# Kernel optimization log

Measured on AMD Instinct MI355X. Metric: run time of the kernel, lower is better.

## Reference

```python
import jax, jax.numpy as jnp
import numpy as np

B, F, H, P, L, A = 8192, 512, 1024, 64, 32, 16


def setup_inputs() -> dict:
    key = jax.random.key(0)
    ks = jax.random.split(key, 7)
    s = lambda k, shape, fan: jax.random.normal(k, shape, jnp.float32) / np.sqrt(fan)
    return {
        "state": jax.random.normal(ks[0], (B, F), jnp.float32),
        "W0": s(ks[1], (A, H, F), F),
        "b0": jnp.zeros((A, H), jnp.float32),
        "W1": s(ks[2], (A, H, H), H),
        "b1": jnp.zeros((A, H), jnp.float32),
        "W2": s(ks[3], (A, P, H), H),
        "ltl_corr": jax.random.normal(ks[4], (A, P), jnp.float32),
        # learned policies = {0..31}; active-only experts = policies 32..47
        "learned_idx": jnp.arange(L, dtype=jnp.int64),
        "active_idx": jnp.arange(L, L + A, dtype=jnp.int64),
    }


def reference(state, W0, b0, W1, b1, W2, ltl_corr, learned_idx, active_idx):
    # Batched over the A active experts (original loops in Python per expert).
    h = jax.nn.relu(jnp.einsum('bf,ahf->abh', state, W0) + b0[:, None, :])   # [A,B,H]
    h = jax.nn.relu(jnp.einsum('abh,agh->abg', h, W1) + b1[:, None, :])      # [A,B,H]
    x = jnp.einsum('abh,aph->abp', h, W2) + ltl_corr[:, None, :]             # [A,B,P]
    # softmax restricted to learned columns, scattered back into zeros
    sub = jax.nn.softmax(x[:, :, learned_idx], axis=-1)                       # [A,B,L]
    emb = jnp.zeros_like(x).at[:, :, learned_idx].set(sub)                    # [A,B,P]
    # all_emb starts as identity per batch element; active rows replaced
    all_emb = jnp.broadcast_to(jnp.eye(P, dtype=state.dtype), (state.shape[0], P, P))
    all_emb = all_emb.at[:, active_idx, :].set(jnp.transpose(emb, (1, 0, 2)))
    return all_emb
```

## Files before the change

### kernel.cpp

```cpp
#include <hip/hip_runtime.h>
#include <hip/hip_bf16.h>


typedef short v8s __attribute__((ext_vector_type(8)));
typedef float v4f __attribute__((ext_vector_type(4)));
using bf16 = __hip_bfloat16;

#define AS_GLOBAL __attribute__((address_space(1)))
#define AS_LDS    __attribute__((address_space(3)))

static constexpr int Mtot = 8192;
static constexpr int Fdim = 512;
static constexpr int Hdim = 1024;
static constexpr int Pdim = 64;
static constexpr int Aexp = 16;

__device__ __forceinline__ void gload_lds16(const void* g, void* l) {
  __builtin_amdgcn_global_load_lds((const AS_GLOBAL void*)g, (AS_LDS void*)l, 16, 0, 0);
}
__device__ __forceinline__ unsigned short bfu(float x) {
  bf16 h = __float2bfloat16(x);
  return *(unsigned short*)&h;
}
#define MFMA16(d, a, b) d = __builtin_amdgcn_mfma_f32_16x16x32_bf16(a, b, d, 0, 0, 0)
#define WAIT_VM3 asm volatile("s_waitcnt vmcnt(3)" ::: "memory")
#define WAIT_VM0 asm volatile("s_waitcnt vmcnt(0)" ::: "memory")
#define BAR() __builtin_amdgcn_s_barrier()

__device__ __forceinline__ void cvt_span(const float* __restrict__ src,
                                         unsigned short* __restrict__ dst, int n4,
                                         int gid, int nthr) {
  for (int i = gid; i < n4; i += nthr) {
    float4 v = ((const float4*)src)[i];
    ushort4 u;
    u.x = bfu(v.x); u.y = bfu(v.y); u.z = bfu(v.z); u.w = bfu(v.w);
    ((ushort4*)dst)[i] = u;
  }
}

__global__ void cvt_all_kernel(const float* __restrict__ s0, unsigned short* __restrict__ d0, int n0,
                               const float* __restrict__ s1, unsigned short* __restrict__ d1, int n1,
                               const float* __restrict__ s2, unsigned short* __restrict__ d2, int n2,
                               const float* __restrict__ s3, unsigned short* __restrict__ d3, int n3) {
  int gid = blockIdx.x * blockDim.x + threadIdx.x;
  int nthr = gridDim.x * blockDim.x;
  cvt_span(s0, d0, n0, gid, nthr);
  cvt_span(s1, d1, n1, gid, nthr);
  cvt_span(s2, d2, n2, gid, nthr);
  cvt_span(s3, d3, n3, gid, nthr);
}

__global__ void ident_kernel(float* __restrict__ outp) {
  const long total4 = (long)Mtot * Pdim * Pdim / 4;
  long i = blockIdx.x * 256 + threadIdx.x;
  const long stride = (long)gridDim.x * 256;
  for (; i < total4; i += stride) {
    long e = i * 4;
    int q = (int)(e & 63);
    int p = (int)((e >> 6) & 63);
    float4 v;
    v.x = (p == q) ? 1.f : 0.f;
    v.y = (p == q + 1) ? 1.f : 0.f;
    v.z = (p == q + 2) ? 1.f : 0.f;
    v.w = (p == q + 3) ? 1.f : 0.f;
    *(float4*)&outp[e] = v;
  }
}

template <int NT>
__global__ __launch_bounds__(256) void gemm97_kernel(
    const bf16* __restrict__ Ain, long aAmul,
    const bf16* __restrict__ Bw,
    const float* __restrict__ bias,
    bf16* __restrict__ Cout, long aCmul, int nbm) {
  constexpr int K = NT * 64;
  __shared__ short lsA[128 * 64];
  __shared__ short lsB[128 * 64];
  const int t = threadIdx.x;
  const int nwg = nbm * 128;

  const int flat = blockIdx.x;
  const int perx = nwg >> 3;
  const int swz = (flat & 7) * perx + (flat >> 3);
  const int perg = nbm * 8;
  const int g = swz / perg;
  const int e = swz % perg;
  const int msup = e >> 5;
  const int ny = (e >> 2) & 7;
  const int mloc = e & 3;
  const int mBase = (msup * 4 + mloc) * 128;
  const int nBase = ny * 128;

  const bf16* A0 = Ain + (size_t)g * aAmul;
  const bf16* B0 = Bw + (size_t)g * (1024 * K);
  const float* biasE = bias + g * 1024 + nBase;
  bf16* C0 = Cout + (size_t)g * aCmul + nBase;

  const int w = t >> 6, lane = t & 63;
  const int wm = w >> 1, wn = w & 1;
  const int lr = lane & 15, lk = lane >> 4;

  v4f acc[4][4];
#pragma unroll
  for (int m = 0; m < 4; ++m)
#pragma unroll
    for (int n = 0; n < 4; ++n) acc[m][n] = (v4f)(0.f);

  const int rowA = t >> 3;
  const int sg = (t & 7) ^ (rowA & 7);
  const bf16* gA = A0 + (size_t)(mBase + rowA) * K + sg * 8;
  const bf16* gB = B0 + (size_t)(nBase + rowA) * K + sg * 8;

  for (int k0 = 0; k0 < K; k0 += 64) {
#pragma unroll
    for (int i = 0; i < 4; ++i) {
      gload_lds16(gA + (size_t)(i * 32) * K + k0, &lsA[i * 2048 + t * 8]);
      gload_lds16(gB + (size_t)(i * 32) * K + k0, &lsB[i * 2048 + t * 8]);
    }
    __syncthreads();
#pragma unroll
    for (int kk = 0; kk < 2; ++kk) {
      v8s af[4], bfr[4];
#pragma unroll
      for (int m = 0; m < 4; ++m) {
        const int row = wm * 64 + m * 16 + lr;
        af[m] = *(const v8s*)&lsA[row * 64 + ((((kk << 2) + lk) ^ (row & 7)) << 3)];
      }
#pragma unroll
      for (int n = 0; n < 4; ++n) {
        const int row = wn * 64 + n * 16 + lr;
        bfr[n] = *(const v8s*)&lsB[row * 64 + ((((kk << 2) + lk) ^ (row & 7)) << 3)];
      }
#pragma unroll
      for (int m = 0; m < 4; ++m)
#pragma unroll
        for (int n = 0; n < 4; ++n)
          MFMA16(acc[m][n], af[m], bfr[n]);
    }
    __syncthreads();
  }

#pragma unroll
  for (int n = 0; n < 4; ++n) {
    const int colIn = wn * 64 + n * 16 + lr;
    const float bv = biasE[colIn];
#pragma unroll
    for (int m = 0; m < 4; ++m) {
      const int row0 = mBase + wm * 64 + m * 16 + lk * 4;
#pragma unroll
      for (int j = 0; j < 4; ++j) {
        float v = acc[m][n][j] + bv;
        v = v > 0.f ? v : 0.f;
        C0[(size_t)(row0 + j) * 1024 + colIn] = __float2bfloat16(v);
      }
    }
  }
}

__global__ __launch_bounds__(256) void gemm2_softmax_kernel(
    const bf16* __restrict__ h1, const bf16* __restrict__ W2b,
    const float* __restrict__ ltl, const int* __restrict__ lidx,
    const int* __restrict__ aidx, float* __restrict__ outp, int mGlobBase, int MC) {
  __shared__ short lsA[2][32 * 64];
  __shared__ short lsB[2][64 * 64];
  __shared__ float X[32][68];
  __shared__ int s_lidx[32];
  __shared__ int s_inv[64];
  __shared__ int s_arow;
  const int a = blockIdx.y;
  const bf16* Ain = h1 + (size_t)a * MC * Hdim;
  const bf16* Bw = W2b + (size_t)a * Pdim * Hdim;
  const float* ltlE = ltl + (size_t)a * Pdim;

  const int t = threadIdx.x;
  const int mBase = blockIdx.x * 32;
  const int w = t >> 6, lane = t & 63;
  const int lr = lane & 15, lk = lane >> 4;
  const int wr = w & 1, wq = w >> 1;

  if (t < 64) s_inv[t] = -1;
  __syncthreads();
  if (t < 32) {
    int q = lidx[t];
    s_lidx[t] = q;
    s_inv[q] = t;
  }
  if (t == 0) s_arow = aidx[a];
  __syncthreads();

  const int srow = t >> 3;
  const int sg = (t & 7) ^ ((t >> 3) & 7);
  const bf16* gA = Ain + (size_t)(mBase + srow) * Hdim + sg * 8;
  const bf16* gB = Bw + (size_t)srow * Hdim + sg * 8;

  auto stage = [&](int buf, int kt) {
    gload_lds16(gA + kt * 64, &lsA[buf][t * 8]);
    gload_lds16(gB + kt * 64, &lsB[buf][t * 8]);
    gload_lds16(gB + (size_t)32 * Hdim + kt * 64, &lsB[buf][2048 + t * 8]);
  };

  v4f acc[2];
  acc[0] = (v4f)(0.f); acc[1] = (v4f)(0.f);

  stage(0, 0);
  for (int kt = 0; kt < 16; ++kt) {
    const int buf = kt & 1;
    if (kt + 1 < 16) { stage(buf ^ 1, kt + 1); WAIT_VM3; } else { WAIT_VM0; }
    BAR();
#pragma unroll
    for (int s = 0; s < 2; ++s) {
      int rowA = wr * 16 + lr;
      v8s af = *(const v8s*)&lsA[buf][rowA * 64 + ((((s << 2) + lk) ^ (rowA & 7)) << 3)];
#pragma unroll
      for (int n = 0; n < 2; ++n) {
        int rowB = wq * 32 + n * 16 + lr;
        v8s bf = *(const v8s*)&lsB[buf][rowB * 64 + ((((s << 2) + lk) ^ (rowB & 7)) << 3)];
        MFMA16(acc[n], af, bf);
      }
    }
    BAR();
  }

#pragma unroll
  for (int n = 0; n < 2; ++n) {
    const int col = wq * 32 + n * 16 + lr;
    const float lc = ltlE[col];
#pragma unroll
    for (int j = 0; j < 4; ++j) {
      X[wr * 16 + lk * 4 + j][col] = acc[n][j] + lc;
    }
  }
  __syncthreads();

  if (t < 32) {
    const int r = t;
    float mx = -1e30f;
#pragma unroll
    for (int l = 0; l < 32; ++l) mx = fmaxf(mx, X[r][s_lidx[l]]);
    float s = 0.f;
#pragma unroll
    for (int l = 0; l < 32; ++l) s += __expf(X[r][s_lidx[l]] - mx);
    const float rs = 1.f / s;
    const size_t obase = ((size_t)(mGlobBase + mBase + r) * 64 + s_arow) * 64;
#pragma unroll
    for (int q0 = 0; q0 < 64; q0 += 4) {
      float4 v;
      v.x = (s_inv[q0 + 0] >= 0) ? __expf(X[r][q0 + 0] - mx) * rs : 0.f;
      v.y = (s_inv[q0 + 1] >= 0) ? __expf(X[r][q0 + 1] - mx) * rs : 0.f;
      v.z = (s_inv[q0 + 2] >= 0) ? __expf(X[r][q0 + 2] - mx) * rs : 0.f;
      v.w = (s_inv[q0 + 3] >= 0) ? __expf(X[r][q0 + 3] - mx) * rs : 0.f;
      *(float4*)&outp[obase + q0] = v;
    }
  }
}

extern "C" void kernel_launch(void* const* d_in, const int* in_sizes, int n_in,
                              void* d_out, int out_size, void* d_ws, size_t ws_size,
                              hipStream_t stream) {
  const float* state = (const float*)d_in[0];
  const float* W0 = (const float*)d_in[1];
  const float* b0 = (const float*)d_in[2];
  const float* W1 = (const float*)d_in[3];
  const float* b1 = (const float*)d_in[4];
  const float* W2 = (const float*)d_in[5];
  const float* ltl = (const float*)d_in[6];
  const int* lidx = (const int*)d_in[7];
  const int* aidx = (const int*)d_in[8];
  float* outp = (float*)d_out;

  char* ws = (char*)d_ws;
  bf16* stateb = (bf16*)ws;
  bf16* W0b = stateb + (size_t)Mtot * Fdim;
  bf16* W1b = W0b + (size_t)Aexp * Hdim * Fdim;
  bf16* W2b = W1b + (size_t)Aexp * Hdim * Hdim;
  bf16* h0 = W2b + (size_t)Aexp * Pdim * Hdim;
  const size_t fixedB = (size_t)(Mtot * Fdim + Aexp * Hdim * Fdim +
                                 Aexp * Hdim * Hdim + Aexp * Pdim * Hdim) * 2;
  int MC = 2048;
  while (MC > 512 && fixedB + (size_t)2 * Aexp * MC * Hdim * 2 + 4096 > ws_size) MC >>= 1;
  bf16* h1 = h0 + (size_t)Aexp * MC * Hdim;

  ident_kernel<<<dim3(4096), dim3(256), 0, stream>>>(outp);
  cvt_all_kernel<<<dim3(2048), dim3(256), 0, stream>>>(
      state, (unsigned short*)stateb, Mtot * Fdim / 4,
      W0, (unsigned short*)W0b, Aexp * Hdim * Fdim / 4,
      W1, (unsigned short*)W1b, Aexp * Hdim * Hdim / 4,
      W2, (unsigned short*)W2b, Aexp * Pdim * Hdim / 4);

  const int nbm = MC / 128;
  for (int mOff = 0; mOff < Mtot; mOff += MC) {
    gemm97_kernel<Fdim / 64><<<dim3(nbm * 128), dim3(256), 0, stream>>>(
        stateb + (size_t)mOff * Fdim, 0L,
        W0b, b0, h0, (long)MC * Hdim, nbm);
    gemm97_kernel<Hdim / 64><<<dim3(nbm * 128), dim3(256), 0, stream>>>(
        h0, (long)MC * Hdim,
        W1b, b1, h1, (long)MC * Hdim, nbm);
    gemm2_softmax_kernel<<<dim3(MC / 32, Aexp), dim3(256), 0, stream>>>(
        h1, W2b, ltl, lidx, aidx, outp, mOff, MC);
  }
}
```

Baseline: 622.5 us.

## Chunk by expert groups instead of batch rows; enlarge gemm2 tile to 128 rows

The host loop now splits the work into groups of G experts covering the full 8192-row batch, where it used to cover all experts over batch chunks. The two large GEMMs now see full-M grids for G experts at a time. The final GEMM+softmax kernel uses 128-row tiles with 2x4 MFMA accumulators per wave and a shared LDS union, so more rows share each W2 tile. The identity fill and the softmax output writes now use nontemporal stores. The gemm97 index math now hardcodes 512 blocks per expert, which ties it to Mtot=8192.

After: 834.9 us. 34.1% more time.

```diff
diff --git a/kernel.cpp b/kernel.cpp
--- a/kernel.cpp
+++ b/kernel.cpp
@@ -23,7 +23,7 @@
   return *(unsigned short*)&h;
 }
 #define MFMA16(d, a, b) d = __builtin_amdgcn_mfma_f32_16x16x32_bf16(a, b, d, 0, 0, 0)
-#define WAIT_VM3 asm volatile("s_waitcnt vmcnt(3)" ::: "memory")
+#define WAIT_VM6 asm volatile("s_waitcnt vmcnt(6)" ::: "memory")
 #define WAIT_VM0 asm volatile("s_waitcnt vmcnt(0)" ::: "memory")
 #define BAR() __builtin_amdgcn_s_barrier()
 
@@ -58,12 +58,12 @@
     long e = i * 4;
     int q = (int)(e & 63);
     int p = (int)((e >> 6) & 63);
-    float4 v;
-    v.x = (p == q) ? 1.f : 0.f;
-    v.y = (p == q + 1) ? 1.f : 0.f;
-    v.z = (p == q + 2) ? 1.f : 0.f;
-    v.w = (p == q + 3) ? 1.f : 0.f;
-    *(float4*)&outp[e] = v;
+    v4f v;
+    v[0] = (p == q) ? 1.f : 0.f;
+    v[1] = (p == q + 1) ? 1.f : 0.f;
+    v[2] = (p == q + 2) ? 1.f : 0.f;
+    v[3] = (p == q + 3) ? 1.f : 0.f;
+    __builtin_nontemporal_store(v, (v4f*)&outp[e]);
   }
 }
 
@@ -72,19 +72,18 @@
     const bf16* __restrict__ Ain, long aAmul,
     const bf16* __restrict__ Bw,
     const float* __restrict__ bias,
-    bf16* __restrict__ Cout, long aCmul, int nbm) {
+    bf16* __restrict__ Cout, long aCmul) {
   constexpr int K = NT * 64;
   __shared__ short lsA[128 * 64];
   __shared__ short lsB[128 * 64];
   const int t = threadIdx.x;
-  const int nwg = nbm * 128;
+  const int nwg = gridDim.x;
 
   const int flat = blockIdx.x;
   const int perx = nwg >> 3;
   const int swz = (flat & 7) * perx + (flat >> 3);
-  const int perg = nbm * 8;
-  const int g = swz / perg;
-  const int e = swz % perg;
+  const int g = swz >> 9;
+  const int e = swz & 511;
   const int msup = e >> 5;
   const int ny = (e >> 2) & 7;
   const int mloc = e & 3;
@@ -160,23 +159,25 @@
 __global__ __launch_bounds__(256) void gemm2_softmax_kernel(
     const bf16* __restrict__ h1, const bf16* __restrict__ W2b,
     const float* __restrict__ ltl, const int* __restrict__ lidx,
-    const int* __restrict__ aidx, float* __restrict__ outp, int mGlobBase, int MC) {
-  __shared__ short lsA[2][32 * 64];
-  __shared__ short lsB[2][64 * 64];
-  __shared__ float X[32][68];
+    const int* __restrict__ aidx, int aOffset, float* __restrict__ outp) {
+  __shared__ char smem[49152];
   __shared__ int s_lidx[32];
   __shared__ int s_inv[64];
   __shared__ int s_arow;
-  const int a = blockIdx.y;
-  const bf16* Ain = h1 + (size_t)a * MC * Hdim;
-  const bf16* Bw = W2b + (size_t)a * Pdim * Hdim;
-  const float* ltlE = ltl + (size_t)a * Pdim;
+  short* lsA = (short*)smem;
+  short* lsB = (short*)(smem + 32768);
+  float(*X)[68] = (float(*)[68])smem;
+
+  const int aLoc = blockIdx.y;
+  const bf16* Ain = h1 + (size_t)aLoc * Mtot * Hdim;
+  const bf16* Bw = W2b + (size_t)aLoc * Pdim * Hdim;
+  const float* ltlE = ltl + (size_t)aLoc * Pdim;
 
   const int t = threadIdx.x;
-  const int mBase = blockIdx.x * 32;
+  const int mBase = blockIdx.x * 128;
   const int w = t >> 6, lane = t & 63;
   const int lr = lane & 15, lk = lane >> 4;
-  const int wr = w & 1, wq = w >> 1;
+  const int wm = w;
 
   if (t < 64) s_inv[t] = -1;
   __syncthreads();
@@ -185,54 +186,69 @@
     s_lidx[t] = q;
     s_inv[q] = t;
   }
-  if (t == 0) s_arow = aidx[a];
+  if (t == 0) s_arow = aidx[aOffset + aLoc];
   __syncthreads();
 
   const int srow = t >> 3;
-  const int sg = (t & 7) ^ ((t >> 3) & 7);
+  const int sg = (t & 7) ^ (srow & 7);
   const bf16* gA = Ain + (size_t)(mBase + srow) * Hdim + sg * 8;
   const bf16* gB = Bw + (size_t)srow * Hdim + sg * 8;
 
   auto stage = [&](int buf, int kt) {
-    gload_lds16(gA + kt * 64, &lsA[buf][t * 8]);
-    gload_lds16(gB + kt * 64, &lsB[buf][t * 8]);
-    gload_lds16(gB + (size_t)32 * Hdim + kt * 64, &lsB[buf][2048 + t * 8]);
+#pragma unroll
+    for (int i = 0; i < 4; ++i)
+      gload_lds16(gA + (size_t)(i * 32) * Hdim + kt * 64, &lsA[buf * 8192 + i * 2048 + t * 8]);
+#pragma unroll
+    for (int i = 0; i < 2; ++i)
+      gload_lds16(gB + (size_t)(i * 32) * Hdim + kt * 64, &lsB[buf * 4096 + i * 2048 + t * 8]);
   };
 
-  v4f acc[2];
-  acc[0] = (v4f)(0.f); acc[1] = (v4f)(0.f);
+  v4f acc[2][4];
+#pragma unroll
+  for (int m = 0; m < 2; ++m)
+#pragma unroll
+    for (int n = 0; n < 4; ++n) acc[m][n] = (v4f)(0.f);
 
   stage(0, 0);
   for (int kt = 0; kt < 16; ++kt) {
     const int buf = kt & 1;
-    if (kt + 1 < 16) { stage(buf ^ 1, kt + 1); WAIT_VM3; } else { WAIT_VM0; }
+    if (kt + 1 < 16) { stage(buf ^ 1, kt + 1); WAIT_VM6; } else { WAIT_VM0; }
     BAR();
 #pragma unroll
-    for (int s = 0; s < 2; ++s) {
-      int rowA = wr * 16 + lr;
-      v8s af = *(const v8s*)&lsA[buf][rowA * 64 + ((((s << 2) + lk) ^ (rowA & 7)) << 3)];
-#pragma unroll
-      for (int n = 0; n < 2; ++n) {
-        int rowB = wq * 32 + n * 16 + lr;
-        v8s bf = *(const v8s*)&lsB[buf][rowB * 64 + ((((s << 2) + lk) ^ (rowB & 7)) << 3)];
-        MFMA16(acc[n], af, bf);
-      }
+    for (int ks = 0; ks < 2; ++ks) {
+      v8s af[2], bfr[4];
+#pragma unroll
+      for (int m = 0; m < 2; ++m) {
+        const int row = wm * 32 + m * 16 + lr;
+        af[m] = *(const v8s*)&lsA[buf * 8192 + row * 64 + ((((ks << 2) + lk) ^ (lr & 7)) << 3)];
+      }
+#pragma unroll
+      for (int n = 0; n < 4; ++n) {
+        const int row = n * 16 + lr;
+        bfr[n] = *(const v8s*)&lsB[buf * 4096 + row * 64 + ((((ks << 2) + lk) ^ (lr & 7)) << 3)];
+      }
+#pragma unroll
+      for (int m = 0; m < 2; ++m)
+#pragma unroll
+        for (int n = 0; n < 4; ++n)
+          MFMA16(acc[m][n], af[m], bfr[n]);
     }
     BAR();
   }
 
 #pragma unroll
-  for (int n = 0; n < 2; ++n) {
-    const int col = wq * 32 + n * 16 + lr;
+  for (int n = 0; n < 4; ++n) {
+    const int col = n * 16 + lr;
     const float lc = ltlE[col];
 #pragma unroll
-    for (int j = 0; j < 4; ++j) {
-      X[wr * 16 + lk * 4 + j][col] = acc[n][j] + lc;
-    }
+    for (int m = 0; m < 2; ++m)
+#pragma unroll
+      for (int j = 0; j < 4; ++j)
+        X[wm * 32 + m * 16 + lk * 4 + j][col] = acc[m][n][j] + lc;
   }
   __syncthreads();
 
-  if (t < 32) {
+  if (t < 128) {
     const int r = t;
     float mx = -1e30f;
 #pragma unroll
@@ -241,15 +257,15 @@
 #pragma unroll
     for (int l = 0; l < 32; ++l) s += __expf(X[r][s_lidx[l]] - mx);
     const float rs = 1.f / s;
-    const size_t obase = ((size_t)(mGlobBase + mBase + r) * 64 + s_arow) * 64;
+    const size_t obase = ((size_t)(mBase + r) * 64 + s_arow) * 64;
 #pragma unroll
     for (int q0 = 0; q0 < 64; q0 += 4) {
-      float4 v;
-      v.x = (s_inv[q0 + 0] >= 0) ? __expf(X[r][q0 + 0] - mx) * rs : 0.f;
-      v.y = (s_inv[q0 + 1] >= 0) ? __expf(X[r][q0 + 1] - mx) * rs : 0.f;
-      v.z = (s_inv[q0 + 2] >= 0) ? __expf(X[r][q0 + 2] - mx) * rs : 0.f;
-      v.w = (s_inv[q0 + 3] >= 0) ? __expf(X[r][q0 + 3] - mx) * rs : 0.f;
-      *(float4*)&outp[obase + q0] = v;
+      v4f v;
+      v[0] = (s_inv[q0 + 0] >= 0) ? __expf(X[r][q0 + 0] - mx) * rs : 0.f;
+      v[1] = (s_inv[q0 + 1] >= 0) ? __expf(X[r][q0 + 1] - mx) * rs : 0.f;
+      v[2] = (s_inv[q0 + 2] >= 0) ? __expf(X[r][q0 + 2] - mx) * rs : 0.f;
+      v[3] = (s_inv[q0 + 3] >= 0) ? __expf(X[r][q0 + 3] - mx) * rs : 0.f;
+      __builtin_nontemporal_store(v, (v4f*)&outp[obase + q0]);
     }
   }
 }
@@ -276,9 +292,10 @@
   bf16* h0 = W2b + (size_t)Aexp * Pdim * Hdim;
   const size_t fixedB = (size_t)(Mtot * Fdim + Aexp * Hdim * Fdim +
                                  Aexp * Hdim * Hdim + Aexp * Pdim * Hdim) * 2;
-  int MC = 2048;
-  while (MC > 512 && fixedB + (size_t)2 * Aexp * MC * Hdim * 2 + 4096 > ws_size) MC >>= 1;
-  bf16* h1 = h0 + (size_t)Aexp * MC * Hdim;
+  int G = 8;
+  while (G > 1 && fixedB + (size_t)2 * G * Mtot * Hdim * 2 + 4096 > ws_size) G >>= 1;
+  bf16* h1 = h0 + (size_t)G * Mtot * Hdim;
+  const int passes = Aexp / G;
 
   ident_kernel<<<dim3(4096), dim3(256), 0, stream>>>(outp);
   cvt_all_kernel<<<dim3(2048), dim3(256), 0, stream>>>(
@@ -287,15 +304,19 @@
       W1, (unsigned short*)W1b, Aexp * Hdim * Hdim / 4,
       W2, (unsigned short*)W2b, Aexp * Pdim * Hdim / 4);
 
-  const int nbm = MC / 128;
-  for (int mOff = 0; mOff < Mtot; mOff += MC) {
-    gemm97_kernel<Fdim / 64><<<dim3(nbm * 128), dim3(256), 0, stream>>>(
-        stateb + (size_t)mOff * Fdim, 0L,
-        W0b, b0, h0, (long)MC * Hdim, nbm);
-    gemm97_kernel<Hdim / 64><<<dim3(nbm * 128), dim3(256), 0, stream>>>(
-        h0, (long)MC * Hdim,
-        W1b, b1, h1, (long)MC * Hdim, nbm);
-    gemm2_softmax_kernel<<<dim3(MC / 32, Aexp), dim3(256), 0, stream>>>(
-        h1, W2b, ltl, lidx, aidx, outp, mOff, MC);
-  }
-}
+  for (int p = 0; p < passes; ++p) {
+    gemm97_kernel<Fdim / 64><<<dim3(512 * G), dim3(256), 0, stream>>>(
+        stateb, 0L,
+        W0b + (size_t)p * G * Hdim * Fdim,
+        b0 + (size_t)p * G * Hdim,
+        h0, (long)Mtot * Hdim);
+    gemm97_kernel<Hdim / 64><<<dim3(512 * G), dim3(256), 0, stream>>>(
+        h0, (long)Mtot * Hdim,
+        W1b + (size_t)p * G * Hdim * Hdim,
+        b1 + (size_t)p * G * Hdim,
+        h1, (long)Mtot * Hdim);
+    gemm2_softmax_kernel<<<dim3(Mtot / 128, G), dim3(256), 0, stream>>>(
+        h1, W2b + (size_t)p * G * Pdim * Hdim,
+        ltl + (size_t)p * G * Pdim, lidx, aidx, p * G, outp);
+  }
+}
```

## Skip identity writes for active rows, use nontemporal stores, enlarge GEMM chunks

Applied to the files above, without the earlier changes.

The identity-fill kernel now builds a bitmask of active expert rows and skips writing those rows, because the softmax kernel overwrites them anyway. Output stores in both kernels become nontemporal. When the workspace is large enough, the first-layer GEMM runs once over the full batch and the second layer plus softmax run in larger chunks, which cuts launch count and improves occupancy per launch. The cost is a larger workspace for the full h0 buffer, and the skip relies on the active index list being read correctly in every thread.

After: 816.2 us. 1.31x slower.

```diff
diff --git a/kernel.cpp b/kernel.cpp
--- a/kernel.cpp
+++ b/kernel.cpp
@@ -50,7 +50,10 @@
   cvt_span(s3, d3, n3, gid, nthr);
 }
 
-__global__ void ident_kernel(float* __restrict__ outp) {
+__global__ void ident_kernel(float* __restrict__ outp, const int* __restrict__ aidx) {
+  unsigned long long act = 0;
+#pragma unroll
+  for (int i = 0; i < Aexp; ++i) act |= 1ull << (aidx[i] & 63);
   const long total4 = (long)Mtot * Pdim * Pdim / 4;
   long i = blockIdx.x * 256 + threadIdx.x;
   const long stride = (long)gridDim.x * 256;
@@ -58,12 +61,13 @@
     long e = i * 4;
     int q = (int)(e & 63);
     int p = (int)((e >> 6) & 63);
-    float4 v;
-    v.x = (p == q) ? 1.f : 0.f;
-    v.y = (p == q + 1) ? 1.f : 0.f;
-    v.z = (p == q + 2) ? 1.f : 0.f;
-    v.w = (p == q + 3) ? 1.f : 0.f;
-    *(float4*)&outp[e] = v;
+    if ((act >> p) & 1) continue;
+    v4f v;
+    v[0] = (p == q) ? 1.f : 0.f;
+    v[1] = (p == q + 1) ? 1.f : 0.f;
+    v[2] = (p == q + 2) ? 1.f : 0.f;
+    v[3] = (p == q + 3) ? 1.f : 0.f;
+    __builtin_nontemporal_store(v, (v4f*)&outp[e]);
   }
 }
 
@@ -244,12 +248,12 @@
     const size_t obase = ((size_t)(mGlobBase + mBase + r) * 64 + s_arow) * 64;
 #pragma unroll
     for (int q0 = 0; q0 < 64; q0 += 4) {
-      float4 v;
-      v.x = (s_inv[q0 + 0] >= 0) ? __expf(X[r][q0 + 0] - mx) * rs : 0.f;
-      v.y = (s_inv[q0 + 1] >= 0) ? __expf(X[r][q0 + 1] - mx) * rs : 0.f;
-      v.z = (s_inv[q0 + 2] >= 0) ? __expf(X[r][q0 + 2] - mx) * rs : 0.f;
-      v.w = (s_inv[q0 + 3] >= 0) ? __expf(X[r][q0 + 3] - mx) * rs : 0.f;
-      *(float4*)&outp[obase + q0] = v;
+      v4f v;
+      v[0] = (s_inv[q0 + 0] >= 0) ? __expf(X[r][q0 + 0] - mx) * rs : 0.f;
+      v[1] = (s_inv[q0 + 1] >= 0) ? __expf(X[r][q0 + 1] - mx) * rs : 0.f;
+      v[2] = (s_inv[q0 + 2] >= 0) ? __expf(X[r][q0 + 2] - mx) * rs : 0.f;
+      v[3] = (s_inv[q0 + 3] >= 0) ? __expf(X[r][q0 + 3] - mx) * rs : 0.f;
+      __builtin_nontemporal_store(v, (v4f*)&outp[obase + q0]);
     }
   }
 }
@@ -276,26 +280,48 @@
   bf16* h0 = W2b + (size_t)Aexp * Pdim * Hdim;
   const size_t fixedB = (size_t)(Mtot * Fdim + Aexp * Hdim * Fdim +
                                  Aexp * Hdim * Hdim + Aexp * Pdim * Hdim) * 2;
-  int MC = 2048;
-  while (MC > 512 && fixedB + (size_t)2 * Aexp * MC * Hdim * 2 + 4096 > ws_size) MC >>= 1;
-  bf16* h1 = h0 + (size_t)Aexp * MC * Hdim;
-
-  ident_kernel<<<dim3(4096), dim3(256), 0, stream>>>(outp);
+  const size_t h0FullB = (size_t)Aexp * Mtot * Hdim * 2;
+
+  bool fullL1 = false;
+  int MCL2 = 4096;
+  if (fixedB + h0FullB + (size_t)Aexp * 4096 * Hdim * 2 + 4096 <= ws_size) {
+    fullL1 = true;
+  } else {
+    MCL2 = 2048;
+    while (MCL2 > 512 &&
+           fixedB + (size_t)2 * Aexp * MCL2 * Hdim * 2 + 4096 > ws_size)
+      MCL2 >>= 1;
+  }
+  bf16* h1 = fullL1 ? h0 + (size_t)Aexp * Mtot * Hdim
+                    : h0 + (size_t)Aexp * MCL2 * Hdim;
+
+  ident_kernel<<<dim3(4096), dim3(256), 0, stream>>>(outp, aidx);
   cvt_all_kernel<<<dim3(2048), dim3(256), 0, stream>>>(
       state, (unsigned short*)stateb, Mtot * Fdim / 4,
       W0, (unsigned short*)W0b, Aexp * Hdim * Fdim / 4,
       W1, (unsigned short*)W1b, Aexp * Hdim * Hdim / 4,
       W2, (unsigned short*)W2b, Aexp * Pdim * Hdim / 4);
 
-  const int nbm = MC / 128;
-  for (int mOff = 0; mOff < Mtot; mOff += MC) {
-    gemm97_kernel<Fdim / 64><<<dim3(nbm * 128), dim3(256), 0, stream>>>(
-        stateb + (size_t)mOff * Fdim, 0L,
-        W0b, b0, h0, (long)MC * Hdim, nbm);
-    gemm97_kernel<Hdim / 64><<<dim3(nbm * 128), dim3(256), 0, stream>>>(
-        h0, (long)MC * Hdim,
-        W1b, b1, h1, (long)MC * Hdim, nbm);
-    gemm2_softmax_kernel<<<dim3(MC / 32, Aexp), dim3(256), 0, stream>>>(
-        h1, W2b, ltl, lidx, aidx, outp, mOff, MC);
-  }
-}
+  if (fullL1) {
+    gemm97_kernel<Fdim / 64><<<dim3((Mtot / 128) * 128), dim3(256), 0, stream>>>(
+        stateb, 0L, W0b, b0, h0, (long)Mtot * Hdim, Mtot / 128);
+    for (int mOff = 0; mOff < Mtot; mOff += MCL2) {
+      gemm97_kernel<Hdim / 64><<<dim3((MCL2 / 128) * 128), dim3(256), 0, stream>>>(
+          h0 + (size_t)mOff * Hdim, (long)Mtot * Hdim,
+          W1b, b1, h1, (long)MCL2 * Hdim, MCL2 / 128);
+      gemm2_softmax_kernel<<<dim3(MCL2 / 32, Aexp), dim3(256), 0, stream>>>(
+          h1, W2b, ltl, lidx, aidx, outp, mOff, MCL2);
+    }
+  } else {
+    for (int mOff = 0; mOff < Mtot; mOff += MCL2) {
+      gemm97_kernel<Fdim / 64><<<dim3((MCL2 / 128) * 128), dim3(256), 0, stream>>>(
+          stateb + (size_t)mOff * Fdim, 0L,
+          W0b, b0, h0, (long)MCL2 * Hdim, MCL2 / 128);
+      gemm97_kernel<Hdim / 64><<<dim3((MCL2 / 128) * 128), dim3(256), 0, stream>>>(
+          h0, (long)MCL2 * Hdim,
+          W1b, b1, h1, (long)MCL2 * Hdim, MCL2 / 128);
+      gemm2_softmax_kernel<<<dim3(MCL2 / 32, Aexp), dim3(256), 0, stream>>>(
+          h1, W2b, ltl, lidx, aidx, outp, mOff, MCL2);
+    }
+  }
+}
```

## Skip identity writes for active rows, use nontemporal stores, shrink M chunk

Applied to the files above, without the earlier changes.

The identity fill kernel now builds a bitmask of the active expert rows and skips writing them, because the softmax kernel overwrites those rows anyway. This removes about a quarter of the 128 MB output write. Both output writers switch to nontemporal stores so the output stream does not evict cached data. The M chunk size is halved from 2048 to 1024, which shrinks the intermediate buffers but doubles the number of GEMM launches.

After: 693.6 us. +11.4%, slower.

```diff
diff --git a/kernel.cpp b/kernel.cpp
--- a/kernel.cpp
+++ b/kernel.cpp
@@ -50,7 +50,10 @@
   cvt_span(s3, d3, n3, gid, nthr);
 }
 
-__global__ void ident_kernel(float* __restrict__ outp) {
+__global__ void ident_kernel(float* __restrict__ outp, const int* __restrict__ aidx) {
+  unsigned long long act = 0;
+#pragma unroll
+  for (int i = 0; i < Aexp; ++i) act |= 1ull << (aidx[i] & 63);
   const long total4 = (long)Mtot * Pdim * Pdim / 4;
   long i = blockIdx.x * 256 + threadIdx.x;
   const long stride = (long)gridDim.x * 256;
@@ -58,12 +61,13 @@
     long e = i * 4;
     int q = (int)(e & 63);
     int p = (int)((e >> 6) & 63);
-    float4 v;
-    v.x = (p == q) ? 1.f : 0.f;
-    v.y = (p == q + 1) ? 1.f : 0.f;
-    v.z = (p == q + 2) ? 1.f : 0.f;
-    v.w = (p == q + 3) ? 1.f : 0.f;
-    *(float4*)&outp[e] = v;
+    if ((act >> p) & 1) continue;
+    v4f v;
+    v[0] = (p == q) ? 1.f : 0.f;
+    v[1] = (p == q + 1) ? 1.f : 0.f;
+    v[2] = (p == q + 2) ? 1.f : 0.f;
+    v[3] = (p == q + 3) ? 1.f : 0.f;
+    __builtin_nontemporal_store(v, (v4f*)&outp[e]);
   }
 }
 
@@ -244,12 +248,12 @@
     const size_t obase = ((size_t)(mGlobBase + mBase + r) * 64 + s_arow) * 64;
 #pragma unroll
     for (int q0 = 0; q0 < 64; q0 += 4) {
-      float4 v;
-      v.x = (s_inv[q0 + 0] >= 0) ? __expf(X[r][q0 + 0] - mx) * rs : 0.f;
-      v.y = (s_inv[q0 + 1] >= 0) ? __expf(X[r][q0 + 1] - mx) * rs : 0.f;
-      v.z = (s_inv[q0 + 2] >= 0) ? __expf(X[r][q0 + 2] - mx) * rs : 0.f;
-      v.w = (s_inv[q0 + 3] >= 0) ? __expf(X[r][q0 + 3] - mx) * rs : 0.f;
-      *(float4*)&outp[obase + q0] = v;
+      v4f v;
+      v[0] = (s_inv[q0 + 0] >= 0) ? __expf(X[r][q0 + 0] - mx) * rs : 0.f;
+      v[1] = (s_inv[q0 + 1] >= 0) ? __expf(X[r][q0 + 1] - mx) * rs : 0.f;
+      v[2] = (s_inv[q0 + 2] >= 0) ? __expf(X[r][q0 + 2] - mx) * rs : 0.f;
+      v[3] = (s_inv[q0 + 3] >= 0) ? __expf(X[r][q0 + 3] - mx) * rs : 0.f;
+      __builtin_nontemporal_store(v, (v4f*)&outp[obase + q0]);
     }
   }
 }
@@ -276,11 +280,11 @@
   bf16* h0 = W2b + (size_t)Aexp * Pdim * Hdim;
   const size_t fixedB = (size_t)(Mtot * Fdim + Aexp * Hdim * Fdim +
                                  Aexp * Hdim * Hdim + Aexp * Pdim * Hdim) * 2;
-  int MC = 2048;
+  int MC = 1024;
   while (MC > 512 && fixedB + (size_t)2 * Aexp * MC * Hdim * 2 + 4096 > ws_size) MC >>= 1;
   bf16* h1 = h0 + (size_t)Aexp * MC * Hdim;
 
-  ident_kernel<<<dim3(4096), dim3(256), 0, stream>>>(outp);
+  ident_kernel<<<dim3(4096), dim3(256), 0, stream>>>(outp, aidx);
   cvt_all_kernel<<<dim3(2048), dim3(256), 0, stream>>>(
       state, (unsigned short*)stateb, Mtot * Fdim / 4,
       W0, (unsigned short*)W0b, Aexp * Hdim * Fdim / 4,
```
